# Kernel optimization log

Hardware: AMD Instinct MI355X
Metric: run time of the kernel (lower is better)

The kernel has to match this reference:

```python
import jax, jax.numpy as jnp
import numpy as np

DIM = 256


def setup_inputs() -> dict:
    key = jax.random.key(0)
    ks = jax.random.split(key, 9)
    B, T, D = 64, 4096, DIM
    s = 1.0 / np.sqrt(D)
    x = jax.random.normal(ks[0], (B, T, D), dtype=jnp.float32)
    Wq = jax.random.uniform(ks[1], (D, D), jnp.float32, -s, s)
    bq = jax.random.uniform(ks[2], (D,), jnp.float32, -s, s)
    Wk = jax.random.uniform(ks[3], (D, D), jnp.float32, -s, s)
    bk = jax.random.uniform(ks[4], (D,), jnp.float32, -s, s)
    Wv = jax.random.uniform(ks[5], (D, D), jnp.float32, -s, s)
    bv = jax.random.uniform(ks[6], (D,), jnp.float32, -s, s)
    Wout = jax.random.uniform(ks[7], (D, 1), jnp.float32, -s, s)
    bout = jax.random.uniform(ks[8], (1,), jnp.float32, -s, s)
    return {"x": x, "Wq": Wq, "bq": bq, "Wk": Wk, "bk": bk,
            "Wv": Wv, "bv": bv, "Wout": Wout, "bout": bout}


def reference(x, Wq, bq, Wk, bk, Wv, bv, Wout, bout):
    # x: [B, T, D]
    q = x[:, -1, :] @ Wq + bq                      # [B, D]
    k = jnp.einsum('btd,de->bte', x, Wk) + bk      # [B, T, D]
    v = jnp.einsum('btd,de->bte', x, Wv) + bv      # [B, T, D]
    # additive (Bahdanau) score: tanh(q + k) projected to scalar
    e = jnp.einsum('btd,d->bt', jnp.tanh(q[:, None, :] + k), Wout[:, 0]) + bout[0]  # [B, T]
    a = jax.nn.softmax(e, axis=-1)                 # [B, T] (dropout = identity in eval)
    return jnp.einsum('bt,btd->bd', a, v)          # [B, D]
```

## Files before the change

### kernel.cpp

```cpp
#include <hip/hip_runtime.h>
#include <hip/hip_bf16.h>

constexpr int DD  = 256;
constexpr int TT  = 4096;
constexpr int NBB = 64;
constexpr int TCC = 32;
constexpr int SPLIT = 8;
constexpr int NCHUNK = (TT / SPLIT) / TCC;
constexpr int CHUNK_BYTES = TCC * DD * 4;

typedef __bf16 bf16_t;
typedef __bf16 bf16x8 __attribute__((ext_vector_type(8)));
typedef float  f32x4  __attribute__((ext_vector_type(4)));

__device__ __forceinline__ float fast_tanh(float x) {
  float e = __expf(x + x);
  return 1.0f - __fdividef(2.0f, e + 1.0f);
}

__device__ __forceinline__ void gload_lds16(const void* g, void* l) {
  __builtin_amdgcn_global_load_lds(
      (const __attribute__((address_space(1))) unsigned int*)g,
      (__attribute__((address_space(3))) unsigned int*)l, 16, 0, 0);
}

__global__ __launch_bounds__(256) void prep_wkT_kernel(
    const float* __restrict__ Wk, unsigned short* __restrict__ wkT) {
  int d = blockIdx.x;
  int n = threadIdx.x;
  union { bf16_t h; unsigned short u; } cv;
  cv.h = (bf16_t)Wk[d * DD + n];
  wkT[n * DD + d] = cv.u;
}

__global__ __launch_bounds__(256) void prep_q_kernel(
    const float* __restrict__ x, const float* __restrict__ Wq,
    const float* __restrict__ bq, const float* __restrict__ bk,
    float* __restrict__ qb2) {
  __shared__ float xl[DD];
  int b = blockIdx.x, tid = threadIdx.x;
  xl[tid] = x[((size_t)b * TT + (TT - 1)) * DD + tid];
  __syncthreads();
  float a = bq[tid] + bk[tid];
  for (int k = 0; k < DD; ++k) a = fmaf(xl[k], Wq[k * DD + tid], a);
  qb2[b * DD + tid] = a;
}

__global__ __launch_bounds__(256, 2) void fused_scores_kernel(
    const float* __restrict__ x, const unsigned short* __restrict__ wkT,
    const float* __restrict__ qb2, const float* __restrict__ wout,
    float* __restrict__ partials) {
  __shared__ __align__(16) char xs[2 * CHUNK_BYTES];
  __shared__ float epart[4 * TCC];
  __shared__ float wbuf[TCC];

  const int tid = threadIdx.x;
  const int b   = blockIdx.y;
  const int bx  = blockIdx.x;
  const int wid = tid >> 6;
  const int l   = tid & 63;
  const int l15 = l & 15;
  const int lg  = l >> 4;

  bf16x8 bfr[4][8];
#pragma unroll
  for (int nt = 0; nt < 4; ++nt) {
    const unsigned short* wp = wkT + (size_t)(wid * 64 + nt * 16 + l15) * DD + lg * 8;
#pragma unroll
    for (int ks = 0; ks < 8; ++ks)
      bfr[nt][ks] = *reinterpret_cast<const bf16x8*>(wp + ks * 32);
  }

  float qcol[4], wcol[4];
#pragma unroll
  for (int nt = 0; nt < 4; ++nt) {
    int col = wid * 64 + nt * 16 + l15;
    qcol[nt] = qb2[b * DD + col];
    wcol[nt] = wout[col];
  }

  const char* xbase =
      (const char*)(x + ((size_t)b * TT + (size_t)bx * (TT / SPLIT)) * DD);

  auto stage = [&](int bufidx, int chunk) {
    const char* xc = xbase + (size_t)chunk * CHUNK_BYTES;
    char* lds = xs + bufidx * CHUNK_BYTES + wid * 8192;
#pragma unroll
    for (int i = 0; i < 8; ++i) {
      int row = wid * 8 + i;
      gload_lds16(xc + row * 1024 + ((l * 16) ^ (i << 4)), lds + i * 1024);
    }
  };

  float s_run = 0.0f, cacc = 0.0f;

  stage(0, 0);
  asm volatile("s_waitcnt vmcnt(0)" ::: "memory");
  __syncthreads();

  for (int j = 0; j < NCHUNK; ++j) {
    const char* xb = xs + (j & 1) * CHUNK_BYTES;
    if (j + 1 < NCHUNK) stage((j + 1) & 1, j + 1);

    f32x4 acc[2][4];
#pragma unroll
    for (int mt = 0; mt < 2; ++mt)
#pragma unroll
      for (int nt = 0; nt < 4; ++nt)
        acc[mt][nt] = f32x4{0.f, 0.f, 0.f, 0.f};

    const int sw = (l15 & 7) << 4;
#pragma unroll
    for (int ks = 0; ks < 8; ++ks) {
      bf16x8 afr[2];
#pragma unroll
      for (int mt = 0; mt < 2; ++mt) {
        int row = mt * 16 + l15;
        const f32x4 a0 = *(const f32x4*)(xb + row * 1024 + ((ks * 128 + lg * 32) ^ sw));
        const f32x4 a1 = *(const f32x4*)(xb + row * 1024 + ((ks * 128 + lg * 32 + 16) ^ sw));
        bf16x8 t;
        t[0] = (bf16_t)a0[0]; t[1] = (bf16_t)a0[1];
        t[2] = (bf16_t)a0[2]; t[3] = (bf16_t)a0[3];
        t[4] = (bf16_t)a1[0]; t[5] = (bf16_t)a1[1];
        t[6] = (bf16_t)a1[2]; t[7] = (bf16_t)a1[3];
        afr[mt] = t;
      }
#pragma unroll
      for (int mt = 0; mt < 2; ++mt)
#pragma unroll
        for (int nt = 0; nt < 4; ++nt)
          acc[mt][nt] = __builtin_amdgcn_mfma_f32_16x16x32_bf16(
              afr[mt], bfr[nt][ks], acc[mt][nt], 0, 0, 0);
    }

    float rs[2][4];
#pragma unroll
    for (int mt = 0; mt < 2; ++mt)
#pragma unroll
      for (int r = 0; r < 4; ++r) rs[mt][r] = 0.0f;
#pragma unroll
    for (int nt = 0; nt < 4; ++nt) {
      float q = qcol[nt], w = wcol[nt];
#pragma unroll
      for (int mt = 0; mt < 2; ++mt)
#pragma unroll
        for (int r = 0; r < 4; ++r)
          rs[mt][r] += fast_tanh(q + acc[mt][nt][r]) * w;
    }
#pragma unroll
    for (int s = 1; s < 16; s <<= 1) {
#pragma unroll
      for (int mt = 0; mt < 2; ++mt)
#pragma unroll
        for (int r = 0; r < 4; ++r)
          rs[mt][r] += __shfl_xor(rs[mt][r], s, 64);
    }
    if (l15 == 0) {
#pragma unroll
      for (int mt = 0; mt < 2; ++mt)
#pragma unroll
        for (int r = 0; r < 4; ++r)
          epart[wid * TCC + mt * 16 + lg * 4 + r] = rs[mt][r];
    }
    __syncthreads();

    if (tid < TCC)
      wbuf[tid] = __expf(epart[tid] + epart[TCC + tid] +
                         epart[2 * TCC + tid] + epart[3 * TCC + tid]);
    __syncthreads();

#pragma unroll 8
    for (int t = 0; t < TCC; ++t) {
      float wt = wbuf[t];
      s_run += wt;
      float xv = *(const float*)(xb + t * 1024 + ((tid * 4) ^ ((t & 7) << 4)));
      cacc = fmaf(wt, xv, cacc);
    }

    asm volatile("s_waitcnt vmcnt(0)" ::: "memory");
    __syncthreads();
  }

  float* p = partials + ((size_t)b * SPLIT + bx) * 257;
  if (tid == 0) p[0] = s_run;
  p[1 + tid] = cacc;
}

__global__ __launch_bounds__(256) void combine_kernel(
    const float* __restrict__ partials, const float* __restrict__ Wv,
    const float* __restrict__ bv, float* __restrict__ out) {
  __shared__ float att[DD];
  int b = blockIdx.x, tid = threadIdx.x;
  const float* pb = partials + (size_t)b * SPLIT * 257;
  float S = 0.0f, C = 0.0f;
  for (int j = 0; j < SPLIT; ++j) {
    S += pb[j * 257];
    C += pb[j * 257 + 1 + tid];
  }
  att[tid] = C;
  __syncthreads();
  float inv = __fdividef(1.0f, S);
  float sum = 0.0f;
  for (int k = 0; k < DD; ++k) sum = fmaf(att[k], Wv[k * DD + tid], sum);
  out[b * DD + tid] = fmaf(sum, inv, bv[tid]);
}

extern "C" void kernel_launch(void* const* d_in, const int* in_sizes, int n_in,
                              void* d_out, int out_size, void* d_ws, size_t ws_size,
                              hipStream_t stream) {
  const float* x    = (const float*)d_in[0];
  const float* Wq   = (const float*)d_in[1];
  const float* bq   = (const float*)d_in[2];
  const float* Wk   = (const float*)d_in[3];
  const float* bk   = (const float*)d_in[4];
  const float* Wv   = (const float*)d_in[5];
  const float* bv   = (const float*)d_in[6];
  const float* Wout = (const float*)d_in[7];
  float* out = (float*)d_out;

  char* ws = (char*)d_ws;
  unsigned short* wkT = (unsigned short*)ws;
  float* qb2      = (float*)(ws + 131072);
  float* partials = (float*)(ws + 131072 + 65536);

  prep_wkT_kernel<<<dim3(256), dim3(256), 0, stream>>>(Wk, wkT);
  prep_q_kernel<<<dim3(64), dim3(256), 0, stream>>>(x, Wq, bq, bk, qb2);
  fused_scores_kernel<<<dim3(SPLIT, NBB), dim3(256), 0, stream>>>(
      x, wkT, qb2, Wout, partials);
  combine_kernel<<<dim3(64), dim3(256), 0, stream>>>(partials, Wv, bv, out);
}
```

Measured before the change: 413.1 us.

## Stage x through registers as bf16 in LDS with 512-thread blocks

Replaces direct global-to-LDS fp32 staging with register loads that convert to bf16 before writing to shared memory. This halves the LDS footprint and read traffic, and removes the repeated per-use fp32-to-bf16 conversion in the MFMA loop. Blocks grow to 8 waves, each owning 32 output columns, and the weighted-sum pass is split across two row halves with a final reduction. The context vector is now accumulated from bf16-rounded x rather than fp32, and the register staging adds VGPR pressure.

```diff
diff --git a/kernel.cpp b/kernel.cpp
--- a/kernel.cpp
+++ b/kernel.cpp
@@ -7,7 +7,7 @@
 constexpr int TCC = 32;
 constexpr int SPLIT = 8;
 constexpr int NCHUNK = (TT / SPLIT) / TCC;
-constexpr int CHUNK_BYTES = TCC * DD * 4;
+constexpr int ROWB = DD * 2;
 
 typedef __bf16 bf16_t;
 typedef __bf16 bf16x8 __attribute__((ext_vector_type(8)));
@@ -16,12 +16,6 @@
 __device__ __forceinline__ float fast_tanh(float x) {
   float e = __expf(x + x);
   return 1.0f - __fdividef(2.0f, e + 1.0f);
-}
-
-__device__ __forceinline__ void gload_lds16(const void* g, void* l) {
-  __builtin_amdgcn_global_load_lds(
-      (const __attribute__((address_space(1))) unsigned int*)g,
-      (__attribute__((address_space(3))) unsigned int*)l, 16, 0, 0);
 }
 
 __global__ __launch_bounds__(256) void prep_wkT_kernel(
@@ -46,13 +40,13 @@
   qb2[b * DD + tid] = a;
 }
 
-__global__ __launch_bounds__(256, 2) void fused_scores_kernel(
+__global__ __launch_bounds__(512, 4) void fused_scores_kernel(
     const float* __restrict__ x, const unsigned short* __restrict__ wkT,
     const float* __restrict__ qb2, const float* __restrict__ wout,
     float* __restrict__ partials) {
-  __shared__ __align__(16) char xs[2 * CHUNK_BYTES];
-  __shared__ float epart[4 * TCC];
-  __shared__ float wbuf[TCC];
+  __shared__ __align__(16) unsigned short xs[2][TCC * DD];
+  __shared__ float epart[8 * TCC];
+  __shared__ float wbuf[TCC + 8];
 
   const int tid = threadIdx.x;
   const int b   = blockIdx.y;
@@ -62,75 +56,79 @@
   const int l15 = l & 15;
   const int lg  = l >> 4;
 
-  bf16x8 bfr[4][8];
-#pragma unroll
-  for (int nt = 0; nt < 4; ++nt) {
-    const unsigned short* wp = wkT + (size_t)(wid * 64 + nt * 16 + l15) * DD + lg * 8;
+  bf16x8 bfr[2][8];
+#pragma unroll
+  for (int nt = 0; nt < 2; ++nt) {
+    const unsigned short* wp =
+        wkT + (size_t)(wid * 32 + nt * 16 + l15) * DD + lg * 8;
 #pragma unroll
     for (int ks = 0; ks < 8; ++ks)
       bfr[nt][ks] = *reinterpret_cast<const bf16x8*>(wp + ks * 32);
   }
 
-  float qcol[4], wcol[4];
-#pragma unroll
-  for (int nt = 0; nt < 4; ++nt) {
-    int col = wid * 64 + nt * 16 + l15;
+  float qcol[2], wcol[2];
+#pragma unroll
+  for (int nt = 0; nt < 2; ++nt) {
+    int col = wid * 32 + nt * 16 + l15;
     qcol[nt] = qb2[b * DD + col];
     wcol[nt] = wout[col];
   }
 
-  const char* xbase =
-      (const char*)(x + ((size_t)b * TT + (size_t)bx * (TT / SPLIT)) * DD);
-
-  auto stage = [&](int bufidx, int chunk) {
-    const char* xc = xbase + (size_t)chunk * CHUNK_BYTES;
-    char* lds = xs + bufidx * CHUNK_BYTES + wid * 8192;
-#pragma unroll
-    for (int i = 0; i < 8; ++i) {
-      int row = wid * 8 + i;
-      gload_lds16(xc + row * 1024 + ((l * 16) ^ (i << 4)), lds + i * 1024);
-    }
+  const float* xc0 = x + ((size_t)b * TT + (size_t)bx * (TT / SPLIT)) * DD;
+
+  float4 r0, r1, r2, r3;
+  auto issue_loads = [&](int chunk) {
+    const float4* p = reinterpret_cast<const float4*>(xc0 + (size_t)chunk * TCC * DD);
+    r0 = p[0 * 512 + tid];
+    r1 = p[1 * 512 + tid];
+    r2 = p[2 * 512 + tid];
+    r3 = p[3 * 512 + tid];
   };
+  auto write_lds = [&](int bufi) {
+    char* base = (char*)xs[bufi];
+    const float4 rr[4] = {r0, r1, r2, r3};
+#pragma unroll
+    for (int i = 0; i < 4; ++i) {
+      int row = i * 8 + wid;
+      union { bf16_t h[4]; uint2 u; } pk;
+      pk.h[0] = (bf16_t)rr[i].x; pk.h[1] = (bf16_t)rr[i].y;
+      pk.h[2] = (bf16_t)rr[i].z; pk.h[3] = (bf16_t)rr[i].w;
+      *reinterpret_cast<uint2*>(base + row * ROWB + ((l * 8) ^ (wid << 4))) = pk.u;
+    }
+  };
 
   float s_run = 0.0f, cacc = 0.0f;
-
-  stage(0, 0);
-  asm volatile("s_waitcnt vmcnt(0)" ::: "memory");
+  const int rh = tid >> 8;
+  const int d  = tid & 255;
+  const int sw = (l15 & 7) << 4;
+
+  issue_loads(0);
+  write_lds(0);
   __syncthreads();
 
   for (int j = 0; j < NCHUNK; ++j) {
-    const char* xb = xs + (j & 1) * CHUNK_BYTES;
-    if (j + 1 < NCHUNK) stage((j + 1) & 1, j + 1);
-
-    f32x4 acc[2][4];
+    const char* xb = (const char*)xs[j & 1];
+    if (j + 1 < NCHUNK) issue_loads(j + 1);
+
+    f32x4 acc[2][2];
 #pragma unroll
     for (int mt = 0; mt < 2; ++mt)
 #pragma unroll
-      for (int nt = 0; nt < 4; ++nt)
+      for (int nt = 0; nt < 2; ++nt)
         acc[mt][nt] = f32x4{0.f, 0.f, 0.f, 0.f};
 
-    const int sw = (l15 & 7) << 4;
 #pragma unroll
     for (int ks = 0; ks < 8; ++ks) {
-      bf16x8 afr[2];
 #pragma unroll
       for (int mt = 0; mt < 2; ++mt) {
         int row = mt * 16 + l15;
-        const f32x4 a0 = *(const f32x4*)(xb + row * 1024 + ((ks * 128 + lg * 32) ^ sw));
-        const f32x4 a1 = *(const f32x4*)(xb + row * 1024 + ((ks * 128 + lg * 32 + 16) ^ sw));
-        bf16x8 t;
-        t[0] = (bf16_t)a0[0]; t[1] = (bf16_t)a0[1];
-        t[2] = (bf16_t)a0[2]; t[3] = (bf16_t)a0[3];
-        t[4] = (bf16_t)a1[0]; t[5] = (bf16_t)a1[1];
-        t[6] = (bf16_t)a1[2]; t[7] = (bf16_t)a1[3];
-        afr[mt] = t;
+        bf16x8 afr = *reinterpret_cast<const bf16x8*>(
+            xb + row * ROWB + ((ks * 64 + lg * 16) ^ sw));
+#pragma unroll
+        for (int nt = 0; nt < 2; ++nt)
+          acc[mt][nt] = __builtin_amdgcn_mfma_f32_16x16x32_bf16(
+              afr, bfr[nt][ks], acc[mt][nt], 0, 0, 0);
       }
-#pragma unroll
-      for (int mt = 0; mt < 2; ++mt)
-#pragma unroll
-        for (int nt = 0; nt < 4; ++nt)
-          acc[mt][nt] = __builtin_amdgcn_mfma_f32_16x16x32_bf16(
-              afr[mt], bfr[nt][ks], acc[mt][nt], 0, 0, 0);
     }
 
     float rs[2][4];
@@ -139,7 +137,7 @@
 #pragma unroll
       for (int r = 0; r < 4; ++r) rs[mt][r] = 0.0f;
 #pragma unroll
-    for (int nt = 0; nt < 4; ++nt) {
+    for (int nt = 0; nt < 2; ++nt) {
       float q = qcol[nt], w = wcol[nt];
 #pragma unroll
       for (int mt = 0; mt < 2; ++mt)
@@ -164,26 +162,41 @@
     }
     __syncthreads();
 
-    if (tid < TCC)
-      wbuf[tid] = __expf(epart[tid] + epart[TCC + tid] +
-                         epart[2 * TCC + tid] + epart[3 * TCC + tid]);
+    if (tid < TCC) {
+      float e = 0.0f;
+#pragma unroll
+      for (int w = 0; w < 8; ++w) e += epart[w * TCC + tid];
+      wbuf[tid] = __expf(e);
+    }
     __syncthreads();
 
-#pragma unroll 8
-    for (int t = 0; t < TCC; ++t) {
-      float wt = wbuf[t];
+#pragma unroll
+    for (int t = 0; t < 16; ++t) {
+      int row = rh * 16 + t;
+      float wt = wbuf[row];
+      unsigned short uh = *reinterpret_cast<const unsigned short*>(
+          xb + row * ROWB + ((d * 2) ^ ((row & 7) << 4)));
+      float xv = __uint_as_float(((unsigned)uh) << 16);
       s_run += wt;
-      float xv = *(const float*)(xb + t * 1024 + ((tid * 4) ^ ((t & 7) << 4)));
       cacc = fmaf(wt, xv, cacc);
     }
 
-    asm volatile("s_waitcnt vmcnt(0)" ::: "memory");
+    if (j + 1 < NCHUNK) write_lds((j + 1) & 1);
     __syncthreads();
   }
 
-  float* p = partials + ((size_t)b * SPLIT + bx) * 257;
-  if (tid == 0) p[0] = s_run;
-  p[1 + tid] = cacc;
+  float* csum = epart;
+  if (rh == 1) {
+    csum[d] = cacc;
+    if (tid == 256) wbuf[TCC] = s_run;
+  }
+  __syncthreads();
+  if (rh == 0) {
+    float ct = cacc + csum[d];
+    float* p = partials + ((size_t)b * SPLIT + bx) * 257;
+    if (tid == 0) p[0] = s_run + wbuf[TCC];
+    p[1 + d] = ct;
+  }
 }
 
 __global__ __launch_bounds__(256) void combine_kernel(
@@ -225,7 +238,7 @@
 
   prep_wkT_kernel<<<dim3(256), dim3(256), 0, stream>>>(Wk, wkT);
   prep_q_kernel<<<dim3(64), dim3(256), 0, stream>>>(x, Wq, bq, bk, qb2);
-  fused_scores_kernel<<<dim3(SPLIT, NBB), dim3(256), 0, stream>>>(
+  fused_scores_kernel<<<dim3(SPLIT, NBB), dim3(512), 0, stream>>>(
       x, wkT, qb2, Wout, partials);
   combine_kernel<<<dim3(64), dim3(256), 0, stream>>>(partials, Wv, bv, out);
 }
```

After: 444.8 us. 1.08x slower.
